# Kernel tuning notes

Measured on AMD Instinct MI355X. Metric: run time of the kernel, lower is better.

The kernel has to match this reference:

```python
import jax, jax.numpy as jnp
import numpy as np

B, N, D, H = 4, 4096, 64, 128
N_STATES = 6
K = 10  # top-k nearest neighbors in detect_basins
EPS = 1e-12


def setup_inputs() -> dict:
    key = jax.random.key(0)
    ks = jax.random.split(key, 12)
    s = 0.05
    return {
        "conformations": jax.random.normal(ks[0], (B, N, D), dtype=jnp.float32),
        "native_state": jax.random.normal(ks[1], (B, D), dtype=jnp.float32),
        # energy net: D -> H -> H//2 -> 1
        "We1": jax.random.normal(ks[2], (D, H), dtype=jnp.float32) * s,
        "be1": jnp.zeros((H,), jnp.float32),
        "We2": jax.random.normal(ks[3], (H, H // 2), dtype=jnp.float32) * s,
        "be2": jnp.zeros((H // 2,), jnp.float32),
        "We3": jax.random.normal(ks[4], (H // 2, 1), dtype=jnp.float32) * s,
        "be3": jnp.zeros((1,), jnp.float32),
        # state classifier: D -> H -> 6
        "Ws1": jax.random.normal(ks[5], (D, H), dtype=jnp.float32) * s,
        "bs1": jnp.zeros((H,), jnp.float32),
        "Ws2": jax.random.normal(ks[6], (H, N_STATES), dtype=jnp.float32) * s,
        "bs2": jnp.zeros((N_STATES,), jnp.float32),
    }


def reference(conformations, native_state, We1, be1, We2, be2, We3, be3, Ws1, bs1, Ws2, bs2):
    relu = jax.nn.relu

    def analyze(conf, native):  # conf: (N, D), native: (D,)
        # predict_energy
        h = relu(conf @ We1 + be1)
        h = relu(h @ We2 + be2)
        e = (h @ We3 + be3)[:, 0]  # (N,)

        # detect_basins: pairwise euclidean distances via Gram trick
        sq = jnp.sum(conf * conf, axis=-1)  # (N,)
        d2 = sq[:, None] + sq[None, :] - 2.0 * (conf @ conf.T)
        dist = jnp.sqrt(jnp.clip(d2, EPS))  # (N, N); eps keeps sqrt grad finite at diag

        negv, idx = jax.lax.top_k(-dist, K)   # ascending distances; idx[:,0] == self
        r = -negv[:, -1]                      # k-th smallest distance per row
        neigh_e = e[idx[:, 1:]]               # (N, K-1) energies of 9 nearest neighbors
        is_basin = jnp.all(e[:, None] <= neigh_e, axis=1)  # local-minimum test

        mask = dist < r[:, None]              # points strictly inside basin radius (incl self)
        depth = jnp.max(jnp.where(mask, e[None, :], -jnp.inf), axis=1) - e
        width = jnp.sum(jnp.where(mask, dist, 0.0), axis=1) / jnp.sum(mask, axis=1)

        # classify_state (computed for every sample; original queries it per basin center)
        logits = relu(conf @ Ws1 + bs1) @ Ws2 + bs2  # (N, 6)

        # compute_funnel_metrics
        nd = jnp.sqrt(jnp.sum((conf - native) ** 2, axis=-1))  # (N,)
        native_energy = e[jnp.argmin(nd)]
        funnel_depth = jnp.max(e) - native_energy
        ruggedness = jnp.std(e, ddof=1)  # torch.std is unbiased
        corr = jnp.corrcoef(jnp.stack([nd, e]))[0, 1]
        se = e[jnp.argsort(nd)]
        frustration = jnp.mean((se[1:] > se[:-1]).astype(jnp.float32))
        metrics = jnp.stack([funnel_depth, ruggedness, corr, frustration, native_energy])
        return e, is_basin, depth, width, logits, metrics

    return jax.vmap(analyze)(conformations, native_state)
```

## Files before the change

kernel.cpp:

```cpp
#include <hip/hip_runtime.h>
#include <float.h>
#include <math.h>

#define NPTS 4096
#define NBATCH 4
#define BN (NBATCH * NPTS)
#define EPSC 1e-12f
#define JS 4
#define CSTRIDE 204
#define NT (NPTS / JS / 64)

typedef __attribute__((ext_vector_type(8))) short bfrag;
typedef __attribute__((ext_vector_type(4))) short bhalf;
typedef __attribute__((ext_vector_type(4))) float f32x4;

#define MFMA(A, B, C) __builtin_amdgcn_mfma_f32_16x16x32_bf16((A), (B), (C), 0, 0, 0)

__device__ __forceinline__ bool dless(float d1, int i1, float d2, int i2) {
  return (d1 < d2) || ((d1 == d2) && (i1 < i2));
}

__device__ __forceinline__ unsigned short f2bf(float x) {
  unsigned b = __float_as_uint(x);
  return (unsigned short)((b + 0x7FFFu + ((b >> 16) & 1u)) >> 16);
}
__device__ __forceinline__ float bf2f(unsigned short u) {
  return __uint_as_float(((unsigned)u) << 16);
}
__device__ __forceinline__ void bf3(float x, unsigned short& u0, unsigned short& u1,
                                    unsigned short& u2) {
  u0 = f2bf(x);
  float r = x - bf2f(u0);
  u1 = f2bf(r);
  r = r - bf2f(u1);
  u2 = f2bf(r);
}

__device__ __forceinline__ void cp16(const void* g, void* l) {
  __builtin_amdgcn_global_load_lds(
      (const __attribute__((address_space(1))) unsigned int*)g,
      (__attribute__((address_space(3))) unsigned int*)l, 16, 0, 0);
}
__device__ __forceinline__ void cp4(const void* g, void* l) {
  __builtin_amdgcn_global_load_lds(
      (const __attribute__((address_space(1))) unsigned int*)g,
      (__attribute__((address_space(3))) unsigned int*)l, 4, 0, 0);
}

__device__ __forceinline__ void gemm32x128(const float (*A)[64], const float* W,
                                           const float* bias, float (*O)[128], int tid) {
  const int pi = (tid >> 5) << 2;
  const int ci = (tid & 31) << 2;
  float acc[4][4] = {};
  for (int k0 = 0; k0 < 64; k0 += 4) {
    alignas(16) float av[4][4], wv[4][4];
#pragma unroll
    for (int r = 0; r < 4; ++r) *(float4*)av[r] = *(const float4*)&A[pi + r][k0];
#pragma unroll
    for (int kk = 0; kk < 4; ++kk) *(float4*)wv[kk] = *(const float4*)&W[(k0 + kk) * 128 + ci];
#pragma unroll
    for (int kk = 0; kk < 4; ++kk)
#pragma unroll
      for (int r = 0; r < 4; ++r)
#pragma unroll
        for (int c = 0; c < 4; ++c)
          acc[r][c] = fmaf(av[r][kk], wv[kk][c], acc[r][c]);
  }
#pragma unroll
  for (int r = 0; r < 4; ++r)
#pragma unroll
    for (int c = 0; c < 4; ++c)
      O[pi + r][ci + c] = fmaxf(acc[r][c] + bias[ci + c], 0.f);
}

__global__ __launch_bounds__(256) void mlp_kernel(
    const float* __restrict__ conf, const float* __restrict__ native,
    const float* __restrict__ We1, const float* __restrict__ be1,
    const float* __restrict__ We2, const float* __restrict__ be2,
    const float* __restrict__ We3, const float* __restrict__ be3,
    const float* __restrict__ Ws1, const float* __restrict__ bs1,
    const float* __restrict__ Ws2, const float* __restrict__ bs2,
    float* __restrict__ e_out, float* __restrict__ logits_out,
    float* __restrict__ sq_ws, float* __restrict__ nd_ws,
    unsigned short* __restrict__ cbf) {
  __shared__ __align__(16) float Wbuf[8192];
  __shared__ __align__(16) float confs[32][64];
  __shared__ __align__(16) float hbuf[32][128];
  __shared__ float nat[64];
  __shared__ float b1s[128], b2s[64], w3s[64], bs1s[128], ws2s[768], bs2s[6];
  __shared__ float be3s;

  const int tid = threadIdx.x;
  const int blk = blockIdx.x;
  const int b = blk >> 7;
  const int pbase = (blk & 127) * 32;
  const float* confb = conf + ((size_t)b * NPTS + pbase) * 64;

  for (int q = tid; q < 512; q += 256) {
    float4 v = *(const float4*)(confb + q * 4);
    *(float4*)&confs[q >> 4][(q & 15) << 2] = v;
  }
  if (tid < 64) nat[tid] = native[b * 64 + tid];
  if (tid < 128) b1s[tid] = be1[tid];
  if (tid < 64) b2s[tid] = be2[tid];
  if (tid < 64) w3s[tid] = We3[tid];
  if (tid < 128) bs1s[tid] = bs1[tid];
  for (int q = tid; q < 768; q += 256) ws2s[q] = Ws2[q];
  if (tid < 6) bs2s[tid] = bs2[tid];
  if (tid == 0) be3s = be3[0];
  for (int q = tid; q < 2048; q += 256)
    *(float4*)&Wbuf[q * 4] = *(const float4*)(Ws1 + q * 4);
  __syncthreads();

  for (int q = tid; q < 512; q += 256) {
    const int pl = q >> 4, k4 = (q & 15) << 2;
    float4 v = *(const float4*)&confs[pl][k4];
    unsigned short x0, x1, x2, y0, y1, y2, z0, z1, z2, w0, w1, w2;
    bf3(v.x, x0, x1, x2);
    bf3(v.y, y0, y1, y2);
    bf3(v.z, z0, z1, z2);
    bf3(v.w, w0, w1, w2);
    unsigned short* dst = cbf + (size_t)(b * NPTS + pbase + pl) * CSTRIDE + k4;
    *(bhalf*)&dst[0] = (bhalf){(short)x0, (short)y0, (short)z0, (short)w0};
    *(bhalf*)&dst[64] = (bhalf){(short)x1, (short)y1, (short)z1, (short)w1};
    *(bhalf*)&dst[128] = (bhalf){(short)x2, (short)y2, (short)z2, (short)w2};
  }

  if (tid < 32) {
    float rs_[8], rn_[8];
#pragma unroll
    for (int u = 0; u < 8; ++u) {
      float c = confs[tid][u];
      rs_[u] = c * c;
      float d = c - nat[u];
      rn_[u] = d * d;
    }
    for (int d0 = 8; d0 < 64; d0 += 8) {
#pragma unroll
      for (int u = 0; u < 8; ++u) {
        float c = confs[tid][d0 + u];
        rs_[u] += c * c;
        float d = c - nat[d0 + u];
        rn_[u] += d * d;
      }
    }
    float s = ((rs_[0] + rs_[1]) + (rs_[2] + rs_[3])) + ((rs_[4] + rs_[5]) + (rs_[6] + rs_[7]));
    float n = ((rn_[0] + rn_[1]) + (rn_[2] + rn_[3])) + ((rn_[4] + rn_[5]) + (rn_[6] + rn_[7]));
    sq_ws[(size_t)b * NPTS + pbase + tid] = s;
    nd_ws[(size_t)b * NPTS + pbase + tid] = sqrtf(n);
  }

  gemm32x128(confs, Wbuf, bs1s, hbuf, tid);
  __syncthreads();

  for (int q = tid; q < 2048; q += 256)
    *(float4*)&Wbuf[q * 4] = *(const float4*)(We1 + q * 4);
  if (tid < 192) {
    int p = tid / 6, s = tid % 6;
    float acc = 0.f;
#pragma unroll 8
    for (int h = 0; h < 128; ++h)
      acc = fmaf(hbuf[p][h], ws2s[h * 6 + s], acc);
    logits_out[((size_t)b * NPTS + pbase + p) * 6 + s] = acc + bs2s[s];
  }
  __syncthreads();

  gemm32x128(confs, Wbuf, b1s, hbuf, tid);
  __syncthreads();

  for (int q = tid; q < 2048; q += 256)
    *(float4*)&Wbuf[q * 4] = *(const float4*)(We2 + q * 4);
  __syncthreads();

  if (tid < 128) {
    const int pi = (tid >> 4) << 2;
    const int ci = (tid & 15) << 2;
    float acc[4][4] = {};
    for (int k0 = 0; k0 < 128; k0 += 4) {
      alignas(16) float av[4][4], wv[4][4];
#pragma unroll
      for (int r = 0; r < 4; ++r) *(float4*)av[r] = *(const float4*)&hbuf[pi + r][k0];
#pragma unroll
      for (int kk = 0; kk < 4; ++kk) *(float4*)wv[kk] = *(const float4*)&Wbuf[(k0 + kk) * 64 + ci];
#pragma unroll
      for (int kk = 0; kk < 4; ++kk)
#pragma unroll
        for (int r = 0; r < 4; ++r)
#pragma unroll
          for (int c = 0; c < 4; ++c)
            acc[r][c] = fmaf(av[r][kk], wv[kk][c], acc[r][c]);
    }
#pragma unroll
    for (int r = 0; r < 4; ++r)
#pragma unroll
      for (int c = 0; c < 4; ++c)
        confs[pi + r][ci + c] = fmaxf(acc[r][c] + b2s[ci + c], 0.f);
  }
  __syncthreads();

  if (tid < 32) {
    float acc = 0.f;
#pragma unroll
    for (int k = 0; k < 64; ++k)
      acc = fmaf(confs[tid][k], w3s[k], acc);
    e_out[(size_t)b * NPTS + pbase + tid] = acc + be3s;
  }
}

__device__ __forceinline__ bfrag ldfrag(const unsigned short* p) {
  bhalf lo = *(const bhalf*)p;
  bhalf hi = *(const bhalf*)(p + 4);
  return __builtin_shufflevector(lo, hi, 0, 1, 2, 3, 4, 5, 6, 7);
}

__device__ __forceinline__ void stage_async(const unsigned short* src,
                                            unsigned short* BU,
                                            const float* sqsrc, float* sqjs,
                                            int tid) {
  const char* s = (const char*)src;
  char* d = (char*)BU;
#pragma unroll
  for (int it = 0; it < 6; ++it) {
    const int q = it * 256 + tid;
    cp16(s + (size_t)q * 16, d + (size_t)q * 16);
  }
  if (tid < 96) {
    const int q = 1536 + tid;
    cp16(s + (size_t)q * 16, d + (size_t)q * 16);
  }
  if (tid < 64) cp4(sqsrc + tid, sqjs + tid);
}

__global__ __launch_bounds__(256, 1) void topk_part_kernel(
    const unsigned short* __restrict__ cbf, const float* __restrict__ sq_ws,
    float* __restrict__ topd, unsigned short* __restrict__ topi) {
  __shared__ __align__(16) unsigned short BU[64 * CSTRIDE];
  __shared__ __align__(16) float Dsf[64 * 68];
  __shared__ float sqjs[64];

  const int tid = threadIdx.x;
  const int b = blockIdx.z;
  const int i0 = blockIdx.x * 64;
  const int jbase = blockIdx.y * (NPTS / JS);
  const unsigned short* cbfb = cbf + (size_t)b * NPTS * CSTRIDE;
  const float* sqb = sq_ws + (size_t)b * NPTS;

  const int l = tid & 63, w = tid >> 6;
  const int cl = l & 15, g = l >> 4;

  const unsigned short* arow = cbfb + (size_t)(i0 + 16 * w + cl) * CSTRIDE + g * 8;
  const bfrag a00 = ldfrag(arow + 0);
  const bfrag a01 = ldfrag(arow + 32);
  const bfrag a10 = ldfrag(arow + 64);
  const bfrag a11 = ldfrag(arow + 96);
  const bfrag a20 = ldfrag(arow + 128);
  const bfrag a21 = ldfrag(arow + 160);
  float sqar[4];
#pragma unroll
  for (int e = 0; e < 4; ++e) sqar[e] = sqb[i0 + 16 * w + 4 * g + e];

  const int irow = tid >> 2, q4 = tid & 3;

  unsigned long long lk[10];
#pragma unroll
  for (int k = 0; k < 10; ++k) lk[k] = 0x7F7FFFFF7FFFFFFFULL;
  float thrf = FLT_MAX;

  stage_async(cbfb + (size_t)jbase * CSTRIDE, BU, sqb + jbase, sqjs, tid);
  __syncthreads();

  for (int jt = 0; jt < NT; ++jt) {
    const int j0 = jbase + jt * 64;

#pragma unroll
    for (int c = 0; c < 4; ++c) {
      const unsigned short* bp = &BU[(16 * c + cl) * CSTRIDE + g * 8];
      const bfrag b00 = ldfrag(bp + 0);
      const bfrag b01 = ldfrag(bp + 32);
      const bfrag b10 = ldfrag(bp + 64);
      const bfrag b11 = ldfrag(bp + 96);
      const bfrag b20 = ldfrag(bp + 128);
      const bfrag b21 = ldfrag(bp + 160);
      f32x4 acc = {0.f, 0.f, 0.f, 0.f};
      acc = MFMA(a00, b00, acc); acc = MFMA(a01, b01, acc);
      acc = MFMA(a00, b10, acc); acc = MFMA(a01, b11, acc);
      acc = MFMA(a10, b00, acc); acc = MFMA(a11, b01, acc);
      acc = MFMA(a00, b20, acc); acc = MFMA(a01, b21, acc);
      acc = MFMA(a10, b10, acc); acc = MFMA(a11, b11, acc);
      acc = MFMA(a20, b00, acc); acc = MFMA(a21, b01, acc);
      const int col = 16 * c + cl;
      const float sj = sqjs[col];
#pragma unroll
      for (int e = 0; e < 4; ++e) {
        const int rw = 16 * w + 4 * g + e;
        float d2 = fmaf(-2.f, acc[e], sqar[e] + sj);
        Dsf[rw * 68 + col] = fmaxf(d2, EPSC);
      }
    }
    __syncthreads();

    if (jt + 1 < NT)
      stage_async(cbfb + (size_t)(j0 + 64) * CSTRIDE, BU, sqb + j0 + 64, sqjs, tid);

    const float* drow = &Dsf[irow * 68 + q4 * 16];
    unsigned mask = 0;
#pragma unroll
    for (int cc = 0; cc < 4; ++cc) {
      float4 v = *(const float4*)&drow[cc * 4];
      mask |= (v.x <= thrf) ? (1u << (cc * 4 + 0)) : 0u;
      mask |= (v.y <= thrf) ? (1u << (cc * 4 + 1)) : 0u;
      mask |= (v.z <= thrf) ? (1u << (cc * 4 + 2)) : 0u;
      mask |= (v.w <= thrf) ? (1u << (cc * 4 + 3)) : 0u;
    }
    const int cnt = __popc(mask);
    int K = cnt;
#pragma unroll
    for (int off = 32; off >= 1; off >>= 1) K = max(K, __shfl_xor(K, off, 64));

    int id = (__ffs(mask) - 1) & 15;
    mask &= mask - 1;
    float dcur = drow[id];
    int jcur = j0 + q4 * 16 + id;
    for (int k = 0; k < K; ++k) {
      const int idn = (__ffs(mask) - 1) & 15;
      mask &= mask - 1;
      const float dnx = drow[idn];
      const int jnx = j0 + q4 * 16 + idn;
      if (k < cnt) {
        unsigned long long cur =
            (((unsigned long long)__float_as_uint(dcur)) << 32) |
            (unsigned long long)(unsigned)jcur;
        if (cur < lk[9]) {
#pragma unroll
          for (int kk = 0; kk < 10; ++kk) {
            bool lt = cur < lk[kk];
            unsigned long long mn = lt ? cur : lk[kk];
            cur = lt ? lk[kk] : cur;
            lk[kk] = mn;
          }
        }
      }
      dcur = dnx;
      jcur = jnx;
    }

    float t = __uint_as_float((unsigned)(lk[9] >> 32));
    t = fminf(t, __shfl_xor(t, 1, 4));
    t = fminf(t, __shfl_xor(t, 2, 4));
    thrf = t;
    __syncthreads();
  }

  float* mrgD = Dsf;
  int* mrgI = (int*)BU;
  {
#pragma unroll
    for (int k = 0; k < 10; ++k) {
      mrgD[irow * 40 + q4 * 10 + k] = __uint_as_float((unsigned)(lk[k] >> 32));
      mrgI[irow * 40 + q4 * 10 + k] = (int)(unsigned)(lk[k] & 0xFFFFFFFFu);
    }
  }
  __syncthreads();
  if (tid < 64) {
    const int base = tid * 40;
    int h0 = 0, h1 = 0, h2 = 0, h3 = 0;
    const size_t obase = (((size_t)b * NPTS + i0 + tid) * JS + blockIdx.y) * 10;
    for (int k = 0; k < 10; ++k) {
      float bd = FLT_MAX; int bi = 0x7fffffff; int bl = -1;
      { float d = mrgD[base + h0];      int ii = mrgI[base + h0];      if (dless(d, ii, bd, bi)) { bd = d; bi = ii; bl = 0; } }
      { float d = mrgD[base + 10 + h1]; int ii = mrgI[base + 10 + h1]; if (dless(d, ii, bd, bi)) { bd = d; bi = ii; bl = 1; } }
      { float d = mrgD[base + 20 + h2]; int ii = mrgI[base + 20 + h2]; if (dless(d, ii, bd, bi)) { bd = d; bi = ii; bl = 2; } }
      { float d = mrgD[base + 30 + h3]; int ii = mrgI[base + 30 + h3]; if (dless(d, ii, bd, bi)) { bd = d; bi = ii; bl = 3; } }
      h0 += (bl == 0); h1 += (bl == 1); h2 += (bl == 2); h3 += (bl == 3);
      topd[obase + k] = bd;
      topi[obase + k] = (unsigned short)bi;
    }
  }
}

__global__ __launch_bounds__(256) void merge_rank_kernel(
    const float* __restrict__ topd, const unsigned short* __restrict__ topi,
    const float* __restrict__ e_in, const float* __restrict__ nd_ws,
    float* __restrict__ basin_out, float* __restrict__ depth_out,
    float* __restrict__ width_out, float* __restrict__ se_ws) {
  __shared__ __align__(16) float ndl[4096];
  const int tid = threadIdx.x;
  if (blockIdx.x < 64) {
    const int g = blockIdx.x * 256 + tid;
    const int b = g >> 12;
    const float* eb = e_in + (size_t)b * NPTS;
    const float* td = topd + (size_t)g * (JS * 10);
    const unsigned short* ti = topi + (size_t)g * (JS * 10);
    const float e_i = eb[g & (NPTS - 1)];
    int h0 = 0, h1 = 0, h2 = 0, h3 = 0;
    float dk[10];
    int ik[10];
#pragma unroll
    for (int k = 0; k < 10; ++k) {
      float bd = FLT_MAX; int bi = 0x7fffffff; int bl = -1;
      { float d = td[h0];      int ii = ti[h0];      if (dless(d, ii, bd, bi)) { bd = d; bi = ii; bl = 0; } }
      { float d = td[10 + h1]; int ii = ti[10 + h1]; if (dless(d, ii, bd, bi)) { bd = d; bi = ii; bl = 1; } }
      { float d = td[20 + h2]; int ii = ti[20 + h2]; if (dless(d, ii, bd, bi)) { bd = d; bi = ii; bl = 2; } }
      { float d = td[30 + h3]; int ii = ti[30 + h3]; if (dless(d, ii, bd, bi)) { bd = d; bi = ii; bl = 3; } }
      h0 += (bl == 0); h1 += (bl == 1); h2 += (bl == 2); h3 += (bl == 3);
      dk[k] = bd;
      ik[k] = bi;
    }
    const float r2 = dk[9];
    bool basin = true;
    float mx = -FLT_MAX, sum = 0.f, cnt = 0.f;
#pragma unroll
    for (int k = 0; k < 10; ++k) {
      float ev = eb[ik[k]];
      if (dk[k] < r2) { mx = fmaxf(mx, ev); sum += sqrtf(dk[k]); cnt += 1.f; }
      if (k >= 1) basin = basin && (e_i <= ev);
    }
    basin_out[g] = basin ? 1.f : 0.f;
    depth_out[g] = mx - e_i;
    width_out[g] = sum / cnt;
  } else {
    const int rb = blockIdx.x - 64;
    const int b = rb >> 6;
    const int i0 = (rb & 63) * 64;
    const float* ndb = nd_ws + (size_t)b * NPTS;
    for (int q = tid; q < 1024; q += 256)
      *(float4*)&ndl[q * 4] = *(const float4*)(ndb + q * 4);
    __syncthreads();
    const int i = i0 + (tid >> 2);
    const int qp = tid & 3;
    const float ndi = ndl[i];
    int rank = 0;
    for (int j = qp * 1024; j < qp * 1024 + 1024; j += 4) {
      float4 v = *(const float4*)&ndl[j];
      rank += (v.x < ndi) || (v.x == ndi && (j + 0) < i);
      rank += (v.y < ndi) || (v.y == ndi && (j + 1) < i);
      rank += (v.z < ndi) || (v.z == ndi && (j + 2) < i);
      rank += (v.w < ndi) || (v.w == ndi && (j + 3) < i);
    }
    rank += __shfl_xor(rank, 1, 4);
    rank += __shfl_xor(rank, 2, 4);
    if (qp == 0) se_ws[(size_t)b * NPTS + rank] = e_in[(size_t)b * NPTS + i];
  }
}

__device__ __forceinline__ float wave_sum(float v) {
#pragma unroll
  for (int off = 32; off >= 1; off >>= 1) v += __shfl_xor(v, off, 64);
  return v;
}
__device__ __forceinline__ float wave_max(float v) {
#pragma unroll
  for (int off = 32; off >= 1; off >>= 1) v = fmaxf(v, __shfl_xor(v, off, 64));
  return v;
}

__global__ __launch_bounds__(1024) void metrics_kernel(
    const float* __restrict__ e_in, const float* __restrict__ nd_ws,
    const float* __restrict__ se_ws, float* __restrict__ metrics_out) {
  __shared__ __align__(16) float el[4096], ndl[4096], sel[4096];
  __shared__ float rA[16], rB[16], rC[16], rD[16], rE[16], rV[16];
  __shared__ int rI[16];
  const int tid = threadIdx.x;
  const int b = blockIdx.x;
  const int wid = tid >> 6, ln = tid & 63;
  const float* eb = e_in + (size_t)b * NPTS;
  const float* ndb = nd_ws + (size_t)b * NPTS;
  const float* seb = se_ws + (size_t)b * NPTS;
  *(float4*)&el[tid * 4] = *(const float4*)(eb + tid * 4);
  *(float4*)&ndl[tid * 4] = *(const float4*)(ndb + tid * 4);
  *(float4*)&sel[tid * 4] = *(const float4*)(seb + tid * 4);
  __syncthreads();

  float pe = 0.f, pnd = 0.f;
  for (int p = tid; p < 4096; p += 1024) { pe += el[p]; pnd += ndl[p]; }
  pe = wave_sum(pe);
  pnd = wave_sum(pnd);
  if (ln == 0) { rA[wid] = pe; rB[wid] = pnd; }
  __syncthreads();
  float me = 0.f, mnd = 0.f;
  for (int i = 0; i < 16; ++i) { me += rA[i]; mnd += rB[i]; }
  me /= 4096.f;
  mnd /= 4096.f;
  __syncthreads();

  float sxx = 0.f, syy = 0.f, sxy = 0.f, mx = -FLT_MAX;
  float bestv = FLT_MAX;
  int besti = 0x7fffffff;
  for (int p = tid; p < 4096; p += 1024) {
    float de = el[p] - me, dn = ndl[p] - mnd;
    syy += de * de;
    sxx += dn * dn;
    sxy += de * dn;
    mx = fmaxf(mx, el[p]);
    if (ndl[p] < bestv || (ndl[p] == bestv && p < besti)) { bestv = ndl[p]; besti = p; }
  }
  float fr = 0.f;
  for (int p = tid; p < 4095; p += 1024) fr += (sel[p + 1] > sel[p]) ? 1.f : 0.f;

  sxx = wave_sum(sxx);
  syy = wave_sum(syy);
  sxy = wave_sum(sxy);
  mx = wave_max(mx);
  fr = wave_sum(fr);
#pragma unroll
  for (int off = 32; off >= 1; off >>= 1) {
    float ov = __shfl_xor(bestv, off, 64);
    int oi = __shfl_xor(besti, off, 64);
    if (ov < bestv || (ov == bestv && oi < besti)) { bestv = ov; besti = oi; }
  }
  if (ln == 0) {
    rA[wid] = sxx; rB[wid] = syy; rC[wid] = sxy;
    rD[wid] = mx;  rE[wid] = fr;  rV[wid] = bestv; rI[wid] = besti;
  }
  __syncthreads();
  if (tid == 0) {
    float tsxx = 0.f, tsyy = 0.f, tsxy = 0.f, tmx = -FLT_MAX, tfr = 0.f;
    float bv = FLT_MAX;
    int bi = 0x7fffffff;
    for (int i = 0; i < 16; ++i) {
      tsxx += rA[i]; tsyy += rB[i]; tsxy += rC[i];
      tmx = fmaxf(tmx, rD[i]); tfr += rE[i];
      if (rV[i] < bv || (rV[i] == bv && rI[i] < bi)) { bv = rV[i]; bi = rI[i]; }
    }
    float ne = el[bi];
    metrics_out[b * 5 + 0] = tmx - ne;
    metrics_out[b * 5 + 1] = sqrtf(tsyy / 4095.f);
    metrics_out[b * 5 + 2] = tsxy / sqrtf(tsxx * tsyy);
    metrics_out[b * 5 + 3] = tfr / 4095.f;
    metrics_out[b * 5 + 4] = ne;
  }
}

extern "C" void kernel_launch(void* const* d_in, const int* in_sizes, int n_in,
                              void* d_out, int out_size, void* d_ws, size_t ws_size,
                              hipStream_t stream) {
  const float* conf = (const float*)d_in[0];
  const float* native = (const float*)d_in[1];
  const float* We1 = (const float*)d_in[2];
  const float* be1 = (const float*)d_in[3];
  const float* We2 = (const float*)d_in[4];
  const float* be2 = (const float*)d_in[5];
  const float* We3 = (const float*)d_in[6];
  const float* be3 = (const float*)d_in[7];
  const float* Ws1 = (const float*)d_in[8];
  const float* bs1 = (const float*)d_in[9];
  const float* Ws2 = (const float*)d_in[10];
  const float* bs2 = (const float*)d_in[11];

  float* out = (float*)d_out;
  float* e_out = out;
  float* basin_out = out + BN;
  float* depth_out = out + 2 * BN;
  float* width_out = out + 3 * BN;
  float* logits_out = out + 4 * BN;
  float* metrics_out = out + 10 * BN;

  float* wsf = (float*)d_ws;
  float* sq_ws = wsf;
  float* nd_ws = wsf + BN;
  float* se_ws = wsf + 2 * (size_t)BN;
  float* topd = wsf + 3 * (size_t)BN;
  unsigned short* topi = (unsigned short*)(wsf + 43 * (size_t)BN);
  unsigned short* cbf = (unsigned short*)(wsf + 63 * (size_t)BN);

  mlp_kernel<<<dim3(512), dim3(256), 0, stream>>>(
      conf, native, We1, be1, We2, be2, We3, be3, Ws1, bs1, Ws2, bs2,
      e_out, logits_out, sq_ws, nd_ws, cbf);
  topk_part_kernel<<<dim3(64, JS, NBATCH), dim3(256), 0, stream>>>(
      cbf, sq_ws, topd, topi);
  merge_rank_kernel<<<dim3(320), dim3(256), 0, stream>>>(
      topd, topi, e_out, nd_ws, basin_out, depth_out, width_out, se_ws);
  metrics_kernel<<<dim3(NBATCH), dim3(1024), 0, stream>>>(e_out, nd_ws, se_ws, metrics_out);
}
```

Measured before the change: 197.0 us.

## Halve row tile per block and split top-k scan across eight lanes per row

Each block of the partial top-k kernel now covers 32 query rows instead of 64, and the grid doubles to 128 blocks in x. Waves split the 64-column tile between them, and eight threads per row each scan eight columns, with an 8-way merge at the end. The goal is more blocks (1024 vs 512) to fill the CUs and shorter per-thread insertion scans. In exchange, each staged B tile is reused by half as many rows, which doubles LDS staging traffic per computed distance, and the final merge has more candidates.

```diff
diff --git a/kernel.cpp b/kernel.cpp
--- a/kernel.cpp
+++ b/kernel.cpp
@@ -235,20 +235,21 @@
     const unsigned short* __restrict__ cbf, const float* __restrict__ sq_ws,
     float* __restrict__ topd, unsigned short* __restrict__ topi) {
   __shared__ __align__(16) unsigned short BU[64 * CSTRIDE];
-  __shared__ __align__(16) float Dsf[64 * 68];
+  __shared__ __align__(16) float Dsf[32 * 68];
   __shared__ float sqjs[64];
 
   const int tid = threadIdx.x;
   const int b = blockIdx.z;
-  const int i0 = blockIdx.x * 64;
+  const int i0 = blockIdx.x * 32;
   const int jbase = blockIdx.y * (NPTS / JS);
   const unsigned short* cbfb = cbf + (size_t)b * NPTS * CSTRIDE;
   const float* sqb = sq_ws + (size_t)b * NPTS;
 
   const int l = tid & 63, w = tid >> 6;
   const int cl = l & 15, g = l >> 4;
-
-  const unsigned short* arow = cbfb + (size_t)(i0 + 16 * w + cl) * CSTRIDE + g * 8;
+  const int rg = w & 1, ch = w >> 1;
+
+  const unsigned short* arow = cbfb + (size_t)(i0 + 16 * rg + cl) * CSTRIDE + g * 8;
   const bfrag a00 = ldfrag(arow + 0);
   const bfrag a01 = ldfrag(arow + 32);
   const bfrag a10 = ldfrag(arow + 64);
@@ -257,9 +258,9 @@
   const bfrag a21 = ldfrag(arow + 160);
   float sqar[4];
 #pragma unroll
-  for (int e = 0; e < 4; ++e) sqar[e] = sqb[i0 + 16 * w + 4 * g + e];
-
-  const int irow = tid >> 2, q4 = tid & 3;
+  for (int e = 0; e < 4; ++e) sqar[e] = sqb[i0 + 16 * rg + 4 * g + e];
+
+  const int irow = tid >> 3, q8 = tid & 7;
 
   unsigned long long lk[10];
 #pragma unroll
@@ -273,8 +274,8 @@
     const int j0 = jbase + jt * 64;
 
 #pragma unroll
-    for (int c = 0; c < 4; ++c) {
-      const unsigned short* bp = &BU[(16 * c + cl) * CSTRIDE + g * 8];
+    for (int c = 0; c < 2; ++c) {
+      const unsigned short* bp = &BU[(32 * ch + 16 * c + cl) * CSTRIDE + g * 8];
       const bfrag b00 = ldfrag(bp + 0);
       const bfrag b01 = ldfrag(bp + 32);
       const bfrag b10 = ldfrag(bp + 64);
@@ -288,11 +289,11 @@
       acc = MFMA(a00, b20, acc); acc = MFMA(a01, b21, acc);
       acc = MFMA(a10, b10, acc); acc = MFMA(a11, b11, acc);
       acc = MFMA(a20, b00, acc); acc = MFMA(a21, b01, acc);
-      const int col = 16 * c + cl;
+      const int col = 32 * ch + 16 * c + cl;
       const float sj = sqjs[col];
 #pragma unroll
       for (int e = 0; e < 4; ++e) {
-        const int rw = 16 * w + 4 * g + e;
+        const int rw = 16 * rg + 4 * g + e;
         float d2 = fmaf(-2.f, acc[e], sqar[e] + sj);
         Dsf[rw * 68 + col] = fmaxf(d2, EPSC);
       }
@@ -302,10 +303,10 @@
     if (jt + 1 < NT)
       stage_async(cbfb + (size_t)(j0 + 64) * CSTRIDE, BU, sqb + j0 + 64, sqjs, tid);
 
-    const float* drow = &Dsf[irow * 68 + q4 * 16];
+    const float* drow = &Dsf[irow * 68 + q8 * 8];
     unsigned mask = 0;
 #pragma unroll
-    for (int cc = 0; cc < 4; ++cc) {
+    for (int cc = 0; cc < 2; ++cc) {
       float4 v = *(const float4*)&drow[cc * 4];
       mask |= (v.x <= thrf) ? (1u << (cc * 4 + 0)) : 0u;
       mask |= (v.y <= thrf) ? (1u << (cc * 4 + 1)) : 0u;
@@ -317,15 +318,15 @@
 #pragma unroll
     for (int off = 32; off >= 1; off >>= 1) K = max(K, __shfl_xor(K, off, 64));
 
-    int id = (__ffs(mask) - 1) & 15;
+    int id = (__ffs(mask) - 1) & 7;
     mask &= mask - 1;
     float dcur = drow[id];
-    int jcur = j0 + q4 * 16 + id;
+    int jcur = j0 + q8 * 8 + id;
     for (int k = 0; k < K; ++k) {
-      const int idn = (__ffs(mask) - 1) & 15;
+      const int idn = (__ffs(mask) - 1) & 7;
       mask &= mask - 1;
       const float dnx = drow[idn];
-      const int jnx = j0 + q4 * 16 + idn;
+      const int jnx = j0 + q8 * 8 + idn;
       if (k < cnt) {
         unsigned long long cur =
             (((unsigned long long)__float_as_uint(dcur)) << 32) |
@@ -345,25 +346,26 @@
     }
 
     float t = __uint_as_float((unsigned)(lk[9] >> 32));
-    t = fminf(t, __shfl_xor(t, 1, 4));
-    t = fminf(t, __shfl_xor(t, 2, 4));
+    t = fminf(t, __shfl_xor(t, 1, 8));
+    t = fminf(t, __shfl_xor(t, 2, 8));
+    t = fminf(t, __shfl_xor(t, 4, 8));
     thrf = t;
     __syncthreads();
   }
 
-  float* mrgD = Dsf;
-  int* mrgI = (int*)BU;
+  float* mrgD = (float*)BU;
+  int* mrgI = (int*)(BU + 5120);
   {
 #pragma unroll
     for (int k = 0; k < 10; ++k) {
-      mrgD[irow * 40 + q4 * 10 + k] = __uint_as_float((unsigned)(lk[k] >> 32));
-      mrgI[irow * 40 + q4 * 10 + k] = (int)(unsigned)(lk[k] & 0xFFFFFFFFu);
-    }
-  }
-  __syncthreads();
-  if (tid < 64) {
-    const int base = tid * 40;
-    int h0 = 0, h1 = 0, h2 = 0, h3 = 0;
+      mrgD[irow * 80 + q8 * 10 + k] = __uint_as_float((unsigned)(lk[k] >> 32));
+      mrgI[irow * 80 + q8 * 10 + k] = (int)(unsigned)(lk[k] & 0xFFFFFFFFu);
+    }
+  }
+  __syncthreads();
+  if (tid < 32) {
+    const int base = tid * 80;
+    int h0 = 0, h1 = 0, h2 = 0, h3 = 0, h4 = 0, h5 = 0, h6 = 0, h7 = 0;
     const size_t obase = (((size_t)b * NPTS + i0 + tid) * JS + blockIdx.y) * 10;
     for (int k = 0; k < 10; ++k) {
       float bd = FLT_MAX; int bi = 0x7fffffff; int bl = -1;
@@ -371,7 +373,12 @@
       { float d = mrgD[base + 10 + h1]; int ii = mrgI[base + 10 + h1]; if (dless(d, ii, bd, bi)) { bd = d; bi = ii; bl = 1; } }
       { float d = mrgD[base + 20 + h2]; int ii = mrgI[base + 20 + h2]; if (dless(d, ii, bd, bi)) { bd = d; bi = ii; bl = 2; } }
       { float d = mrgD[base + 30 + h3]; int ii = mrgI[base + 30 + h3]; if (dless(d, ii, bd, bi)) { bd = d; bi = ii; bl = 3; } }
+      { float d = mrgD[base + 40 + h4]; int ii = mrgI[base + 40 + h4]; if (dless(d, ii, bd, bi)) { bd = d; bi = ii; bl = 4; } }
+      { float d = mrgD[base + 50 + h5]; int ii = mrgI[base + 50 + h5]; if (dless(d, ii, bd, bi)) { bd = d; bi = ii; bl = 5; } }
+      { float d = mrgD[base + 60 + h6]; int ii = mrgI[base + 60 + h6]; if (dless(d, ii, bd, bi)) { bd = d; bi = ii; bl = 6; } }
+      { float d = mrgD[base + 70 + h7]; int ii = mrgI[base + 70 + h7]; if (dless(d, ii, bd, bi)) { bd = d; bi = ii; bl = 7; } }
       h0 += (bl == 0); h1 += (bl == 1); h2 += (bl == 2); h3 += (bl == 3);
+      h4 += (bl == 4); h5 += (bl == 5); h6 += (bl == 6); h7 += (bl == 7);
       topd[obase + k] = bd;
       topi[obase + k] = (unsigned short)bi;
     }
@@ -566,7 +573,7 @@
   mlp_kernel<<<dim3(512), dim3(256), 0, stream>>>(
       conf, native, We1, be1, We2, be2, We3, be3, Ws1, bs1, Ws2, bs2,
       e_out, logits_out, sq_ws, nd_ws, cbf);
-  topk_part_kernel<<<dim3(64, JS, NBATCH), dim3(256), 0, stream>>>(
+  topk_part_kernel<<<dim3(128, JS, NBATCH), dim3(256), 0, stream>>>(
       cbf, sq_ws, topd, topi);
   merge_rank_kernel<<<dim3(320), dim3(256), 0, stream>>>(
       topd, topi, e_out, nd_ws, basin_out, depth_out, width_out, se_ws);
```

Measured after the change: 278.3 us. 41.2% more time.
